# Performance work log

Measured on AMD Instinct MI355X. Metric: run time of the kernel, lower is better.

Reference implementation:

```python
import jax, jax.numpy as jnp
import numpy as np

N, E, D, H, C, G = 20000, 160000, 128, 4, 3, 512
IN_F, EF = 74, 11


def setup_inputs():
    key = jax.random.key(0)
    ks = jax.random.split(key, 20)
    rn = lambda k, shape, s=0.05: jax.random.normal(k, shape, jnp.float32) * s
    return {
        "h0": rn(ks[0], (N, IN_F), 1.0),
        "e_f": rn(ks[1], (E, EF), 1.0),
        "src": jax.random.randint(ks[2], (E,), 0, N, jnp.int32),
        "dst": jax.random.randint(ks[3], (E,), 0, N, jnp.int32),
        "node_gid": jnp.sort(jax.random.randint(ks[4], (N,), 0, G, jnp.int32)),
        "num_graphs": G,
        "lin0_W": rn(ks[5], (H, IN_F, D)),
        "lin_W": rn(ks[6], (C - 1, H, D, D)),
        "We_W": rn(ks[7], (C, H, EF, D)),
        "Wq_W": rn(ks[8], (C, H, D, D)),
        "Wk_W": rn(ks[9], (C, H, D, D)),
        "Wv_W": rn(ks[10], (C, H, D, D)),
        "ln_g": jnp.ones((C, H, D), jnp.float32),
        "ln_b": jnp.zeros((C, H, D), jnp.float32),
        "out_W": rn(ks[11], (C, H * D, D)),
        "out_b": jnp.zeros((C, D), jnp.float32),
        "proj_W": rn(ks[12], (IN_F, D)),
        "proj_b": jnp.zeros((D,), jnp.float32),
        "gru_Wih0": rn(ks[13], (2, D, 3 * D)),
        "gru_Whh0": rn(ks[14], (2, D, 3 * D)),
        "gru_bih0": jnp.zeros((2, 3 * D), jnp.float32),
        "gru_bhh0": jnp.zeros((2, 3 * D), jnp.float32),
        "gru_Wih1": rn(ks[15], (2, 2 * D, 3 * D)),
        "gru_Whh1": rn(ks[16], (2, D, 3 * D)),
        "gru_bih1": jnp.zeros((2, 3 * D), jnp.float32),
        "gru_bhh1": jnp.zeros((2, 3 * D), jnp.float32),
    }


def _seg_mean(x, ids, n):
    s = jax.ops.segment_sum(x, ids, num_segments=n)
    c = jax.ops.segment_sum(jnp.ones((x.shape[0], 1), x.dtype), ids, num_segments=n)
    return s / jnp.maximum(c, 1.0)


def _layernorm(x, g, b, eps=1e-5):
    m = jnp.mean(x, -1, keepdims=True)
    v = jnp.var(x, -1, keepdims=True)
    return (x - m) * jax.lax.rsqrt(v + eps) * g + b


def _gat_head(h, ef_raw, src, dst, n, Wl, We, Wq, Wk, Wv, g, b):
    z = h @ Wl                                  # [N, D]
    ef = ef_raw @ We                            # [E, D]
    x = jnp.stack([z[src], z[dst], ef], axis=1)  # [E, 3, D]
    Q = jnp.einsum('eid,df->eif', x, Wq)
    K = jnp.einsum('eid,df->eif', x, Wk)
    V = jnp.einsum('eid,df->eif', x, Wv)
    attn = jax.nn.softmax(jnp.einsum('eid,ejd->eij', Q, K), axis=-1)  # [E,3,3]
    m = jnp.einsum('eij,ejd->ed', attn, V)      # (attn @ V).sum(1)
    h_new = _seg_mean(m, dst, n)                # mean over incoming edges
    return _layernorm(jax.nn.relu(h_new), g, b)


def _gru_dir(xs, Wih, Whh, bih, bhh, reverse):
    # xs: [T, B, in]; torch gate order r, z, n
    def step(h, x):
        gi = x @ Wih + bih
        gh = h @ Whh + bhh
        ir, iz, inn = jnp.split(gi, 3, axis=-1)
        hr, hz, hn = jnp.split(gh, 3, axis=-1)
        r = jax.nn.sigmoid(ir + hr)
        zg = jax.nn.sigmoid(iz + hz)
        ng = jnp.tanh(inn + r * hn)
        h_new = (1.0 - zg) * ng + zg * h
        return h_new, h_new
    h0 = jnp.zeros((xs.shape[1], Whh.shape[0]), xs.dtype)
    hT, ys = jax.lax.scan(step, h0, xs, reverse=reverse)
    return hT, ys


def _forward(h0, e_f, lin0_W, lin_W, We_W, Wq_W, Wk_W, Wv_W, ln_g, ln_b,
             out_W, out_b, proj_W, proj_b,
             gru_Wih0, gru_Whh0, gru_bih0, gru_bhh0,
             gru_Wih1, gru_Whh1, gru_bih1, gru_bhh1,
             src, dst, node_gid, num_graphs):
    n = h0.shape[0]
    conv_nums, head_nums = We_W.shape[0], We_W.shape[1]
    gru_list = [_seg_mean(h0, node_gid, num_graphs)]
    h = h0
    for j in range(conv_nums):
        heads = [_gat_head(h, e_f, src, dst, n,
                           lin0_W[i] if j == 0 else lin_W[j - 1, i],
                           We_W[j, i], Wq_W[j, i], Wk_W[j, i], Wv_W[j, i],
                           ln_g[j, i], ln_b[j, i])
                 for i in range(head_nums)]
        h = jnp.concatenate(heads, axis=1) @ out_W[j] + out_b[j]
        gru_list.append(_seg_mean(h, node_gid, num_graphs))
    # GRU readout: project initial 74-dim readout, seq = [proj, h1..hC]
    x0 = gru_list[0] @ proj_W + proj_b
    seq = jnp.stack([x0] + gru_list[1:], axis=0)  # [T, G, D]
    hf0, yf0 = _gru_dir(seq, gru_Wih0[0], gru_Whh0[0], gru_bih0[0], gru_bhh0[0], False)
    hb0, yb0 = _gru_dir(seq, gru_Wih0[1], gru_Whh0[1], gru_bih0[1], gru_bhh0[1], True)
    seq1 = jnp.concatenate([yf0, yb0], axis=-1)   # [T, G, 2D]
    hf1, _ = _gru_dir(seq1, gru_Wih1[0], gru_Whh1[0], gru_bih1[0], gru_bhh1[0], False)
    hb1, _ = _gru_dir(seq1, gru_Wih1[1], gru_Whh1[1], gru_bih1[1], gru_bhh1[1], True)
    # torch returns sum over the [num_layers*2, G, D] final hidden stack
    return hf0 + hb0 + hf1 + hb1


def reference(h0, e_f, src, dst, node_gid, num_graphs, lin0_W, lin_W, We_W,
              Wq_W, Wk_W, Wv_W, ln_g, ln_b, out_W, out_b, proj_W, proj_b,
              gru_Wih0, gru_Whh0, gru_bih0, gru_bhh0,
              gru_Wih1, gru_Whh1, gru_bih1, gru_bhh1):
    return _forward(h0, e_f, lin0_W, lin_W, We_W, Wq_W, Wk_W, Wv_W, ln_g, ln_b,
                    out_W, out_b, proj_W, proj_b,
                    gru_Wih0, gru_Whh0, gru_bih0, gru_bhh0,
                    gru_Wih1, gru_Whh1, gru_bih1, gru_bhh1,
                    src, dst, node_gid, num_graphs)
```

## Files before the change

kernel.cpp:

```cpp
#include <hip/hip_runtime.h>
#include <cstdint>

#define D_   128
#define H_   4
#define C_   3
#define G_   512
#define INF_ 74
#define EF_  11
#define T_   4
#define NW_  48

typedef __attribute__((ext_vector_type(8))) short bf16x8;
typedef __attribute__((ext_vector_type(4))) float f32x4;

__device__ inline unsigned short f2bf(float x) {
  unsigned u = __float_as_uint(x);
  unsigned r = u + 0x7fffu + ((u >> 16) & 1u);
  return (unsigned short)(r >> 16);
}
__device__ inline float bf2f(unsigned short x) {
  return __uint_as_float(((unsigned)x) << 16);
}
__device__ inline void unpack8(uint4 u, float* f) {
  f[0] = __uint_as_float(u.x << 16); f[1] = __uint_as_float(u.x & 0xffff0000u);
  f[2] = __uint_as_float(u.y << 16); f[3] = __uint_as_float(u.y & 0xffff0000u);
  f[4] = __uint_as_float(u.z << 16); f[5] = __uint_as_float(u.z & 0xffff0000u);
  f[6] = __uint_as_float(u.w << 16); f[7] = __uint_as_float(u.w & 0xffff0000u);
}

struct WDesc { const float* src; unsigned short* dst; int K; int D; int trans; };
struct WPack { WDesc d[NW_]; };

__global__ __launch_bounds__(256) void k_wcvt(WPack wp)
{
  WDesc w = wp.d[blockIdx.y];
  int tot = w.K * w.D;
  for (int i = blockIdx.x * 256 + threadIdx.x; i < tot; i += gridDim.x * 256) {
    if (w.trans) {
      int d = i / w.K, k = i - d * w.K;
      w.dst[i] = f2bf(w.src[(size_t)k * w.D + d]);
    } else {
      w.dst[i] = f2bf(w.src[i]);
    }
  }
}

__global__ __launch_bounds__(256) void k_bcw(
    const float* __restrict__ GqT, const float* __restrict__ GcT,
    unsigned short* __restrict__ UTBt)
{
  int ch = blockIdx.x;
  unsigned short* dst = UTBt + (size_t)ch * 49152 + 32768;
  const float* gq = GqT + (size_t)ch * EF_ * 128;
  const float* gc = GcT + (size_t)ch * EF_ * 128;
  for (int i = threadIdx.x; i < 16384; i += 256) {
    int r = i >> 7, k = i & 127;
    float v = (r < EF_) ? gq[r * 128 + k]
            : (r < 2 * EF_) ? gc[(r - EF_) * 128 + k] : 0.f;
    dst[i] = f2bf(v);
  }
}

template <typename AT>
__global__ __launch_bounds__(256) void k_mfma(
    const AT* __restrict__ A, int lda, int aOffZ, int M, int K,
    const unsigned short* __restrict__ Bt, int btOffY, int btOffZ,
    float* __restrict__ outF, int ldc, int cOffY, int cOffZ,
    const float* __restrict__ bias,
    unsigned short* __restrict__ outH, int hStride, int hOffY, int hOffZ)
{
  const int bx = blockIdx.x, by = blockIdx.y, bz = blockIdx.z;
  A += (size_t)bz * aOffZ;
  const unsigned short* Bp = Bt + (size_t)by * btOffY + (size_t)bz * btOffZ;
  const int rowBase = bx * 128;
  __shared__ unsigned short As[128][40];
  __shared__ unsigned short Bs[128][40];
  const int t = threadIdx.x;
  const int w = t >> 6, l = t & 63;
  const int wr = w >> 1, wc = w & 1;
  const int fr = l & 15, fq = l >> 4;
  f32x4 acc[4][4];
#pragma unroll
  for (int m = 0; m < 4; m++)
#pragma unroll
    for (int n = 0; n < 4; n++) acc[m][n] = (f32x4){0.f, 0.f, 0.f, 0.f};

  const int sr = t >> 1, sh = t & 1;
  const int arow = rowBase + sr;
  const AT* aBase = A + (size_t)arow * lda;

  for (int k0 = 0; k0 < K; k0 += 32) {
    int kb = k0 + sh * 16;
    if constexpr (sizeof(AT) == 4) {
      unsigned short tmp[16];
      if (arow < M && kb + 16 <= K) {
        const AT* ap = aBase + kb;
#pragma unroll
        for (int i = 0; i < 16; i++) tmp[i] = f2bf(ap[i]);
      } else {
#pragma unroll
        for (int i = 0; i < 16; i++) {
          int gk = kb + i;
          float v = (arow < M && gk < K) ? (float)aBase[gk] : 0.f;
          tmp[i] = f2bf(v);
        }
      }
      *(uint4*)&As[sr][sh * 16]     = *(const uint4*)&tmp[0];
      *(uint4*)&As[sr][sh * 16 + 8] = *(const uint4*)&tmp[8];
    } else {
      if (arow < M && kb + 16 <= K) {
        const unsigned short* ap = (const unsigned short*)aBase + kb;
        *(uint4*)&As[sr][sh * 16]     = *(const uint4*)(ap);
        *(uint4*)&As[sr][sh * 16 + 8] = *(const uint4*)(ap + 8);
      } else {
#pragma unroll
        for (int i = 0; i < 16; i++) {
          int gk = kb + i;
          As[sr][sh * 16 + i] = (arow < M && gk < K)
              ? ((const unsigned short*)aBase)[gk] : (unsigned short)0;
        }
      }
    }
    if (t < 128) {
      unsigned short tmp[32];
      if (k0 + 32 <= K) {
        const unsigned short* bp = Bp + (size_t)t * K + k0;
#pragma unroll
        for (int i = 0; i < 32; i++) tmp[i] = bp[i];
      } else {
#pragma unroll
        for (int i = 0; i < 32; i++) {
          int gk = k0 + i;
          tmp[i] = (gk < K) ? Bp[(size_t)t * K + gk] : (unsigned short)0;
        }
      }
#pragma unroll
      for (int i = 0; i < 4; i++) *(uint4*)&Bs[t][i * 8] = *(const uint4*)&tmp[i * 8];
    }
    __syncthreads();
    bf16x8 af[4], bfr[4];
#pragma unroll
    for (int m = 0; m < 4; m++) af[m]  = *(const bf16x8*)&As[wr * 64 + m * 16 + fr][fq * 8];
#pragma unroll
    for (int n = 0; n < 4; n++) bfr[n] = *(const bf16x8*)&Bs[wc * 64 + n * 16 + fr][fq * 8];
#pragma unroll
    for (int m = 0; m < 4; m++)
#pragma unroll
      for (int n = 0; n < 4; n++)
        acc[m][n] = __builtin_amdgcn_mfma_f32_16x16x32_bf16(af[m], bfr[n], acc[m][n], 0, 0, 0);
    __syncthreads();
  }
#pragma unroll
  for (int m = 0; m < 4; m++) {
    int row0 = rowBase + wr * 64 + m * 16 + fq * 4;
#pragma unroll
    for (int n = 0; n < 4; n++) {
      int col = wc * 64 + n * 16 + fr;
#pragma unroll
      for (int r = 0; r < 4; r++) {
        int row = row0 + r;
        if (row < M) {
          float v = acc[m][n][r];
          if (outH) {
            outH[(size_t)row * hStride + by * hOffY + bz * hOffZ + col] = f2bf(v);
          } else {
            if (bias) v += bias[col];
            outF[(size_t)row * ldc + by * cOffY + bz * cOffZ + col] = v;
          }
        }
      }
    }
  }
}

__global__ void k_hist(const int* __restrict__ dst, int* __restrict__ deg, int E)
{
  int e = blockIdx.x * blockDim.x + threadIdx.x;
  if (e < E) atomicAdd(&deg[dst[e]], 1);
}

__global__ __launch_bounds__(1024) void k_scan(const int* __restrict__ deg,
                                               int* __restrict__ rowp, int N)
{
  __shared__ int part[1024];
  int t = threadIdx.x;
  int chunk = (N + 1023) / 1024;
  int base = t * chunk;
  int s = 0;
  for (int i = 0; i < chunk; i++) { int idx = base + i; if (idx < N) s += deg[idx]; }
  part[t] = s;
  __syncthreads();
  for (int off = 1; off < 1024; off <<= 1) {
    int v = (t >= off) ? part[t - off] : 0;
    __syncthreads();
    part[t] += v;
    __syncthreads();
  }
  int run = part[t] - s;
  for (int i = 0; i < chunk; i++) {
    int idx = base + i;
    if (idx < N) { rowp[idx] = run; run += deg[idx]; }
  }
  if (t == 1023) rowp[N] = part[1023];
}

__global__ void k_fill(const int* __restrict__ src, const int* __restrict__ dst,
                       const int* __restrict__ rowp, int* __restrict__ cursor,
                       int* __restrict__ eids, int* __restrict__ src_perm,
                       int* __restrict__ dst_perm, int E)
{
  int e = blockIdx.x * blockDim.x + threadIdx.x;
  if (e < E) {
    int d = dst[e];
    int pos = atomicAdd(&cursor[d], 1);
    int slot = rowp[d] + pos;
    eids[slot] = e;
    src_perm[slot] = src[e];
    dst_perm[slot] = d;
  }
}

__global__ void k_efperm(const float* __restrict__ e_f, const int* __restrict__ eids,
                         float* __restrict__ ef_perm, int E)
{
  int i = blockIdx.x * blockDim.x + threadIdx.x;
  if (i < E * EF_) {
    int idx = i / EF_, f = i - idx * EF_;
    ef_perm[i] = e_f[(size_t)eids[idx] * EF_ + f];
  }
}

__global__ __launch_bounds__(128) void k_small(
    const float* __restrict__ WeW, const float* __restrict__ WqW,
    const float* __restrict__ WkW, const float* __restrict__ WvW,
    float* __restrict__ WeQ, float* __restrict__ WeK, float* __restrict__ WeV,
    float* __restrict__ M2, float* __restrict__ GqT, float* __restrict__ GcT)
{
  int ch = blockIdx.x;
  const float* We = WeW + (size_t)ch * EF_ * 128;
  const float* Wq = WqW + (size_t)ch * 128 * 128;
  const float* Wk = WkW + (size_t)ch * 128 * 128;
  const float* Wv = WvW + (size_t)ch * 128 * 128;
  __shared__ float sWe[EF_ * 128], sQ[EF_ * 128], sK[EF_ * 128];
  int d = threadIdx.x;
  for (int i = d; i < EF_ * 128; i += 128) sWe[i] = We[i];
  __syncthreads();
  for (int f = 0; f < EF_; f++) {
    float aq = 0.f, ak = 0.f, av = 0.f;
    for (int k = 0; k < 128; k++) {
      float w = sWe[f * 128 + k];
      aq += w * Wq[k * 128 + d];
      ak += w * Wk[k * 128 + d];
      av += w * Wv[k * 128 + d];
    }
    WeQ[(size_t)ch * EF_ * 128 + f * 128 + d] = aq;
    WeK[(size_t)ch * EF_ * 128 + f * 128 + d] = ak;
    WeV[(size_t)ch * EF_ * 128 + f * 128 + d] = av;
    sQ[f * 128 + d] = aq;
    sK[f * 128 + d] = ak;
  }
  __syncthreads();
  if (d < EF_ * EF_) {
    int a = d / EF_, b = d % EF_;
    float s = 0.f;
    for (int k = 0; k < 128; k++) s += sQ[a * 128 + k] * sK[b * 128 + k];
    M2[(size_t)ch * (EF_ * EF_) + d] = s;
  }
  for (int f = 0; f < EF_; f++) {
    float aq = 0.f, ac = 0.f;
    for (int k = 0; k < 128; k++) {
      aq += Wq[(size_t)d * 128 + k] * sK[f * 128 + k];
      ac += Wk[(size_t)d * 128 + k] * sQ[f * 128 + k];
    }
    GqT[(size_t)ch * EF_ * 128 + f * 128 + d] = aq;
    GcT[(size_t)ch * EF_ * 128 + f * 128 + d] = ac;
  }
}

__global__ __launch_bounds__(128) void k_wve(
    const float* __restrict__ WvW, const float* __restrict__ WeV,
    unsigned short* __restrict__ WvE)
{
  int ch = blockIdx.x;
  const float* Wv  = WvW + (size_t)ch * 16384;
  const float* wev = WeV + (size_t)ch * EF_ * 128;
  unsigned short* dst = WvE + (size_t)ch * 20480;
  for (int i = threadIdx.x; i < 20480; i += 128) {
    int d = i / 160, k = i - d * 160;
    float v = (k < 128) ? Wv[(size_t)k * 128 + d]
            : (k < 128 + EF_) ? wev[(size_t)(k - 128) * 128 + d] : 0.f;
    dst[i] = f2bf(v);
  }
}

__global__ __launch_bounds__(256) void k_ss(
    const unsigned short* __restrict__ Zb, const unsigned short* __restrict__ UTb,
    float* __restrict__ ss, int N)
{
  int h = threadIdx.x >> 6, lane = threadIdx.x & 63;
  int n = blockIdx.x;
  unsigned uz = *(const unsigned*)(Zb + (size_t)n * 512 + h * 128 + 2 * lane);
  unsigned uu = *(const unsigned*)(UTb + (size_t)n * 1536 + h * 384 + 2 * lane);
  float zx = __uint_as_float(uz << 16), zy = __uint_as_float(uz & 0xffff0000u);
  float ux = __uint_as_float(uu << 16), uy = __uint_as_float(uu & 0xffff0000u);
  float p = zx * ux + zy * uy;
#pragma unroll
  for (int m = 32; m; m >>= 1) p += __shfl_xor(p, m, 64);
  if (lane == 0) ss[n * H_ + h] = p;
}

__global__ __launch_bounds__(256) void k_elog(
    const unsigned short* __restrict__ UTb, const float* __restrict__ ss,
    const float* __restrict__ M2, const float* __restrict__ ef_perm,
    const int* __restrict__ src_perm, const int* __restrict__ dst_perm,
    float* __restrict__ elog, int E, int layer)
{
  int i0 = blockIdx.x * 64;
  __shared__ float efs[64 * EF_];
  __shared__ float m2s[4 * EF_ * EF_];
  int t = threadIdx.x;
  for (int i = t; i < 64 * EF_; i += 256) {
    int gi = i0 * EF_ + i;
    efs[i] = (gi < E * EF_) ? ef_perm[gi] : 0.f;
  }
  for (int i = t; i < 4 * EF_ * EF_; i += 256)
    m2s[i] = M2[(size_t)layer * 4 * EF_ * EF_ + i];
  __syncthreads();
  int sl = t >> 2, h = t & 3;
  int idx = i0 + sl;
  if (idx < E) {
    int s = src_perm[idx], d = dst_perm[idx];
    const float* ef = &efs[sl * EF_];
    const float* m2 = &m2s[h * EF_ * EF_];
    float ee = 0.f;
#pragma unroll
    for (int a = 0; a < EF_; a++) {
      float r = 0.f;
#pragma unroll
      for (int b = 0; b < EF_; b++) r += m2[a * EF_ + b] * ef[b];
      ee += ef[a] * r;
    }
    const unsigned short* bs = UTb + (size_t)s * 1536 + h * 384 + 256;
    const unsigned short* cs = bs + EF_;
    const unsigned short* bd = UTb + (size_t)d * 1536 + h * 384 + 256;
    const unsigned short* cd = bd + EF_;
    float se = 0.f, es = 0.f, de = 0.f, ed = 0.f;
#pragma unroll
    for (int f = 0; f < EF_; f++) {
      float e = ef[f];
      se += bf2f(bs[f]) * e;
      es += bf2f(cs[f]) * e;
      de += bf2f(bd[f]) * e;
      ed += bf2f(cd[f]) * e;
    }
    float* o = elog + ((size_t)idx * H_ + h) * 6;
    o[0] = ss[s * H_ + h];
    o[1] = se; o[2] = de; o[3] = es; o[4] = ed; o[5] = ee;
  }
}

__global__ __launch_bounds__(256) void k_edge(
    const unsigned short* __restrict__ Zb, const unsigned short* __restrict__ UTb,
    const float* __restrict__ ss, const float* __restrict__ elog,
    const float* __restrict__ ef_perm, const int* __restrict__ rowp,
    const int* __restrict__ src_perm, unsigned short* __restrict__ aggZE, int N)
{
  const int h = threadIdx.x >> 6;
  const int lane = threadIdx.x & 63;
  const int q = lane & 15;
  const int g = lane >> 4;
  const int lb = lane & 48;
  const int n = blockIdx.x;

  float zd[8], ud[8], td[8];
  unpack8(*(const uint4*)(Zb + (size_t)n * 512 + h * 128 + q * 8), zd);
  const unsigned short* utp = UTb + (size_t)n * 1536 + h * 384 + q * 8;
  unpack8(*(const uint4*)(utp), ud);
  unpack8(*(const uint4*)(utp + 128), td);
  const float ssd = ss[n * H_ + h];
  const int beg = rowp[n], end = rowp[n + 1];
  float acc[8];
#pragma unroll
  for (int i = 0; i < 8; i++) acc[i] = 0.f;
  float wdsum = 0.f, a11 = 0.f;

  for (int idx0 = beg; idx0 < end; idx0 += 4) {
    int idxg = idx0 + g;
    bool act = idxg < end;
    int idxc = act ? idxg : beg;
    int s = src_perm[idxc];
    float zs[8];
    unpack8(*(const uint4*)(Zb + (size_t)s * 512 + h * 128 + q * 8), zs);
    float v1 = 0.f, v2 = 0.f;
#pragma unroll
    for (int i = 0; i < 8; i++) {
      v1 += zs[i] * ud[i];
      v2 += zs[i] * td[i];
    }
#pragma unroll
    for (int m = 1; m < 16; m <<= 1) {
      v1 += __shfl_xor(v1, m, 64);
      v2 += __shfl_xor(v2, m, 64);
    }
    float lv = (q < 6) ? elog[((size_t)idxc * H_ + h) * 6 + q] : 0.f;
    float S00 = __shfl(lv, lb + 0, 64);
    float S02 = __shfl(lv, lb + 1, 64);
    float S12 = __shfl(lv, lb + 2, 64);
    float S20 = __shfl(lv, lb + 3, 64);
    float S21 = __shfl(lv, lb + 4, 64);
    float S22 = __shfl(lv, lb + 5, 64);
    float m0 = fmaxf(fmaxf(S00, v1), S02);
    float e00 = __expf(S00 - m0), e01 = __expf(v1 - m0), e02 = __expf(S02 - m0);
    float i0r = 1.f / (e00 + e01 + e02);
    float m1 = fmaxf(fmaxf(v2, ssd), S12);
    float e10 = __expf(v2 - m1), e11 = __expf(ssd - m1), e12 = __expf(S12 - m1);
    float i1r = 1.f / (e10 + e11 + e12);
    float m2 = fmaxf(fmaxf(S20, S21), S22);
    float e20 = __expf(S20 - m2), e21 = __expf(S21 - m2), e22 = __expf(S22 - m2);
    float i2r = 1.f / (e20 + e21 + e22);
    float w0 = e00 * i0r + e10 * i1r + e20 * i2r;
    float w1 = e01 * i0r + e11 * i1r + e21 * i2r;
    float w2 = e02 * i0r + e12 * i1r + e22 * i2r;
    if (!act) { w0 = 0.f; w1 = 0.f; w2 = 0.f; }
#pragma unroll
    for (int i = 0; i < 8; i++) acc[i] += w0 * zs[i];
    wdsum += w1;
    float efl = (q < EF_) ? ef_perm[(size_t)idxc * EF_ + q] : 0.f;
    a11 += w2 * efl;
  }
#pragma unroll
  for (int m = 16; m < 64; m <<= 1) {
#pragma unroll
    for (int i = 0; i < 8; i++) acc[i] += __shfl_xor(acc[i], m, 64);
    wdsum += __shfl_xor(wdsum, m, 64);
    a11 += __shfl_xor(a11, m, 64);
  }
  int cnt = end - beg;
  float invc = (cnt > 0) ? 1.f / (float)cnt : 1.f;
  unsigned short* ob = aggZE + (size_t)n * 640 + h * 160;
  if (g == 0) {
    unsigned short tmp[8];
#pragma unroll
    for (int i = 0; i < 8; i++) tmp[i] = f2bf((acc[i] + wdsum * zd[i]) * invc);
    *(uint4*)(ob + q * 8) = *(const uint4*)&tmp[0];
    ob[128 + q] = (q < EF_) ? f2bf(a11 * invc) : (unsigned short)0;
  } else if (g == 1) {
    ob[144 + q] = 0;
  }
}

__global__ __launch_bounds__(256) void k_ln(
    float* __restrict__ zh, const float* __restrict__ lng,
    const float* __restrict__ lnb, int N, int layer)
{
  int h = threadIdx.x >> 6, lane = threadIdx.x & 63;
  int n = blockIdx.x;
  float* p = zh + (size_t)n * 512 + h * 128 + 2 * lane;
  float2 v = *(const float2*)p;
  v.x = fmaxf(v.x, 0.f); v.y = fmaxf(v.y, 0.f);
  float s1 = v.x + v.y;
#pragma unroll
  for (int m = 32; m; m >>= 1) s1 += __shfl_xor(s1, m, 64);
  float mean = s1 * (1.f / 128.f);
  float dx = v.x - mean, dy = v.y - mean;
  float s2 = dx * dx + dy * dy;
#pragma unroll
  for (int m = 32; m; m >>= 1) s2 += __shfl_xor(s2, m, 64);
  float rstd = rsqrtf(s2 * (1.f / 128.f) + 1e-5f);
  int gi = (layer * H_ + h) * 128 + 2 * lane;
  float2 g2 = *(const float2*)&lng[gi];
  float2 b2 = *(const float2*)&lnb[gi];
  float2 o;
  o.x = dx * rstd * g2.x + b2.x;
  o.y = dy * rstd * g2.y + b2.y;
  *(float2*)p = o;
}

__global__ void k_gmean(const float* __restrict__ X, const int* __restrict__ gid,
                        float* __restrict__ outp, int N, int ld)
{
  int g = blockIdx.x;
  int lo = 0, hi = N;
  while (lo < hi) { int m = (lo + hi) >> 1; if (gid[m] < g) lo = m + 1; else hi = m; }
  int s0 = lo;
  lo = s0; hi = N;
  while (lo < hi) { int m = (lo + hi) >> 1; if (gid[m] < g + 1) lo = m + 1; else hi = m; }
  int s1 = lo;
  float inv = 1.f / (float)((s1 - s0) > 0 ? (s1 - s0) : 1);
  for (int d = threadIdx.x; d < ld; d += blockDim.x) {
    float s = 0.f;
    for (int n = s0; n < s1; n++) s += X[(size_t)n * ld + d];
    outp[(size_t)g * ld + d] = s * inv;
  }
}

__global__ __launch_bounds__(128) void k_gru(
    const float* __restrict__ seq, int inDim,
    const float* __restrict__ Wih, const float* __restrict__ Whh,
    const float* __restrict__ bih, const float* __restrict__ bhh,
    float* __restrict__ yout, float* __restrict__ hfinal)
{
  int g = blockIdx.x, dir = blockIdx.y, d = threadIdx.x;
  const float* Wih_d = Wih + (size_t)dir * inDim * 384;
  const float* Whh_d = Whh + (size_t)dir * 128 * 384;
  const float* bih_d = bih + dir * 384;
  const float* bhh_d = bhh + dir * 384;
  __shared__ float xb[256];
  __shared__ float hb[128];
  float h = 0.f;
  for (int st = 0; st < T_; st++) {
    int t = dir ? (T_ - 1 - st) : st;
    for (int k = d; k < inDim; k += 128) xb[k] = seq[((size_t)t * G_ + g) * inDim + k];
    hb[d] = h;
    __syncthreads();
    float gr = bih_d[d], gz = bih_d[128 + d], gn = bih_d[256 + d];
    for (int k = 0; k < inDim; k++) {
      float xv = xb[k];
      const float* wr = Wih_d + (size_t)k * 384;
      gr += xv * wr[d];
      gz += xv * wr[128 + d];
      gn += xv * wr[256 + d];
    }
    float hr = bhh_d[d], hz = bhh_d[128 + d], hn = bhh_d[256 + d];
    for (int k = 0; k < 128; k++) {
      float hv = hb[k];
      const float* wr = Whh_d + (size_t)k * 384;
      hr += hv * wr[d];
      hz += hv * wr[128 + d];
      hn += hv * wr[256 + d];
    }
    float r  = 1.f / (1.f + __expf(-(gr + hr)));
    float zg = 1.f / (1.f + __expf(-(gz + hz)));
    float ng = tanhf(gn + r * hn);
    h = (1.f - zg) * ng + zg * h;
    if (yout) yout[((size_t)t * G_ + g) * 256 + dir * 128 + d] = h;
    __syncthreads();
  }
  hfinal[((size_t)dir * G_ + g) * 128 + d] = h;
}

__global__ void k_final(const float* __restrict__ fp, float* __restrict__ outp, int n)
{
  int i = blockIdx.x * blockDim.x + threadIdx.x;
  if (i < n) {
    outp[i] = fp[i] + fp[G_ * 128 + i] + fp[2 * G_ * 128 + i] + fp[3 * G_ * 128 + i];
  }
}

extern "C" void kernel_launch(void* const* d_in, const int* in_sizes, int n_in,
                              void* d_out, int out_size, void* d_ws, size_t ws_size,
                              hipStream_t stream)
{
  (void)n_in; (void)ws_size;
  const float* h0   = (const float*)d_in[0];
  const float* e_f  = (const float*)d_in[1];
  const int*   srcI = (const int*)d_in[2];
  const int*   dstI = (const int*)d_in[3];
  const int*   gid  = (const int*)d_in[4];
  const float* lin0 = (const float*)d_in[6];
  const float* linW = (const float*)d_in[7];
  const float* WeW  = (const float*)d_in[8];
  const float* WqW  = (const float*)d_in[9];
  const float* WkW  = (const float*)d_in[10];
  const float* WvW  = (const float*)d_in[11];
  const float* lng  = (const float*)d_in[12];
  const float* lnb  = (const float*)d_in[13];
  const float* outW = (const float*)d_in[14];
  const float* outb = (const float*)d_in[15];
  const float* projW= (const float*)d_in[16];
  const float* projb= (const float*)d_in[17];
  const float* Wih0 = (const float*)d_in[18];
  const float* Whh0 = (const float*)d_in[19];
  const float* bih0 = (const float*)d_in[20];
  const float* bhh0 = (const float*)d_in[21];
  const float* Wih1 = (const float*)d_in[22];
  const float* Whh1 = (const float*)d_in[23];
  const float* bih1 = (const float*)d_in[24];
  const float* bhh1 = (const float*)d_in[25];
  float* outp = (float*)d_out;

  const int N = in_sizes[0] / INF_;
  const int E = in_sizes[2];

  char* wp = (char*)d_ws;
  auto alloc = [&](size_t bytes) -> void* {
    void* p = (void*)wp;
    wp += (bytes + 255) & ~(size_t)255;
    return p;
  };
  unsigned short* Zb  = (unsigned short*)alloc((size_t)N * 512 * 2);
  unsigned short* UTb = (unsigned short*)alloc((size_t)N * 1536 * 2);
  unsigned short* aggZE = (unsigned short*)alloc((size_t)N * 640 * 2);
  float* zh   = (float*)alloc((size_t)N * 512 * 4);
  float* hcur = (float*)alloc((size_t)N * 128 * 4);
  float* ssb  = (float*)alloc((size_t)N * H_ * 4);
  float* elog = (float*)alloc((size_t)E * H_ * 6 * 4);
  float* efp  = (float*)alloc((size_t)E * EF_ * 4);
  float* WeQ  = (float*)alloc((size_t)C_ * H_ * EF_ * 128 * 4);
  float* WeK  = (float*)alloc((size_t)C_ * H_ * EF_ * 128 * 4);
  float* WeV  = (float*)alloc((size_t)C_ * H_ * EF_ * 128 * 4);
  float* M2   = (float*)alloc((size_t)C_ * H_ * EF_ * EF_ * 4);
  float* GqT  = (float*)alloc((size_t)C_ * H_ * EF_ * 128 * 4);
  float* GcT  = (float*)alloc((size_t)C_ * H_ * EF_ * 128 * 4);
  float* Mbuf = (float*)alloc((size_t)C_ * H_ * 16384 * 4);
  unsigned short* WkPl  = (unsigned short*)alloc((size_t)C_ * H_ * 16384 * 2);
  unsigned short* UTBt  = (unsigned short*)alloc((size_t)C_ * H_ * 3 * 16384 * 2);
  unsigned short* WvE   = (unsigned short*)alloc((size_t)C_ * H_ * 20480 * 2);
  unsigned short* linBt0 = (unsigned short*)alloc((size_t)4 * 128 * INF_ * 2);
  unsigned short* linBt12= (unsigned short*)alloc((size_t)2 * 512 * 128 * 2);
  unsigned short* outBt  = (unsigned short*)alloc((size_t)C_ * 128 * 512 * 2);
  unsigned short* projBt = (unsigned short*)alloc((size_t)128 * INF_ * 2);
  int* deg    = (int*)alloc((size_t)N * 4);
  int* cursor = (int*)alloc((size_t)N * 4);
  int* rowp   = (int*)alloc((size_t)(N + 1) * 4);
  int* eids   = (int*)alloc((size_t)E * 4);
  int* srcp   = (int*)alloc((size_t)E * 4);
  int* dstp   = (int*)alloc((size_t)E * 4);
  float* gm74 = (float*)alloc((size_t)G_ * INF_ * 4);
  float* seq  = (float*)alloc((size_t)T_ * G_ * 128 * 4);
  float* seq1 = (float*)alloc((size_t)T_ * G_ * 256 * 4);
  float* fparts=(float*)alloc((size_t)4 * G_ * 128 * 4);

  const int gM = (N + 127) / 128;

  hipMemsetAsync(deg, 0, (size_t)N * 4, stream);
  hipMemsetAsync(cursor, 0, (size_t)N * 4, stream);
  k_hist<<<(E + 255) / 256, 256, 0, stream>>>(dstI, deg, E);
  k_scan<<<1, 1024, 0, stream>>>(deg, rowp, N);
  k_fill<<<(E + 255) / 256, 256, 0, stream>>>(srcI, dstI, rowp, cursor,
                                              eids, srcp, dstp, E);
  k_efperm<<<(E * EF_ + 255) / 256, 256, 0, stream>>>(e_f, eids, efp, E);

  k_small<<<C_ * H_, 128, 0, stream>>>(WeW, WqW, WkW, WvW, WeQ, WeK, WeV, M2,
                                       GqT, GcT);
  k_wve<<<C_ * H_, 128, 0, stream>>>(WvW, WeV, WvE);

  {
    WPack w{};
    int nw = 0;
    auto addw = [&](const float* s, unsigned short* d, int K, int D, int tr) {
      w.d[nw].src = s; w.d[nw].dst = d; w.d[nw].K = K; w.d[nw].D = D;
      w.d[nw].trans = tr; nw++;
    };
    for (int h = 0; h < 4; h++)
      addw(lin0 + (size_t)h * INF_ * 128, linBt0 + (size_t)h * 128 * INF_, INF_, 128, 1);
    for (int j = 1; j < 3; j++)
      for (int h = 0; h < 4; h++)
        addw(linW + ((size_t)(j - 1) * 4 + h) * 16384,
             linBt12 + (size_t)(j - 1) * 65536 + (size_t)h * 16384, 128, 128, 1);
    for (int j = 0; j < 3; j++)
      addw(outW + (size_t)j * 65536, outBt + (size_t)j * 65536, 512, 128, 1);
    addw(projW, projBt, INF_, 128, 1);
    for (int ch = 0; ch < 12; ch++)
      addw(WkW + (size_t)ch * 16384, WkPl + (size_t)ch * 16384, 128, 128, 0);
    k_wcvt<<<dim3(64, nw), 256, 0, stream>>>(w);
  }

  k_mfma<float><<<dim3(1, 1, 12), 256, 0, stream>>>(
      WqW, 128, 16384, 128, 128, WkPl, 0, 16384,
      Mbuf, 128, 0, 16384, nullptr, nullptr, 0, 0, 0);

  {
    WPack w{};
    int nw = 0;
    for (int ch = 0; ch < 12; ch++) {
      w.d[nw++] = { Mbuf + (size_t)ch * 16384, UTBt + (size_t)ch * 49152,
                    128, 128, 0 };
      w.d[nw++] = { Mbuf + (size_t)ch * 16384, UTBt + (size_t)ch * 49152 + 16384,
                    128, 128, 1 };
    }
    k_wcvt<<<dim3(64, nw), 256, 0, stream>>>(w);
    k_bcw<<<12, 256, 0, stream>>>(GqT, GcT, UTBt);
  }

  k_gmean<<<G_, 128, 0, stream>>>(h0, gid, gm74, N, INF_);
  k_mfma<float><<<dim3(4, 1, 1), 256, 0, stream>>>(
      gm74, INF_, 0, G_, INF_, projBt, 0, 0,
      seq, 128, 0, 0, projb, nullptr, 0, 0, 0);

  for (int j = 0; j < C_; j++) {
    if (j == 0)
      k_mfma<float><<<dim3(gM, 4, 1), 256, 0, stream>>>(
          h0, INF_, 0, N, INF_, linBt0, 128 * INF_, 0,
          nullptr, 0, 0, 0, nullptr, Zb, 512, 128, 0);
    else
      k_mfma<float><<<dim3(gM, 4, 1), 256, 0, stream>>>(
          hcur, 128, 0, N, 128, linBt12 + (size_t)(j - 1) * 65536, 16384, 0,
          nullptr, 0, 0, 0, nullptr, Zb, 512, 128, 0);
    k_mfma<unsigned short><<<dim3(gM, 3, 4), 256, 0, stream>>>(
        Zb, 512, 128, N, 128, UTBt + (size_t)j * 4 * 49152, 16384, 49152,
        nullptr, 0, 0, 0, nullptr, UTb, 1536, 128, 384);
    k_ss<<<N, 256, 0, stream>>>(Zb, UTb, ssb, N);
    k_elog<<<(E + 63) / 64, 256, 0, stream>>>(UTb, ssb, M2, efp, srcp, dstp,
                                              elog, E, j);
    k_edge<<<N, 256, 0, stream>>>(Zb, UTb, ssb, elog, efp, rowp, srcp, aggZE, N);
    k_mfma<unsigned short><<<dim3(gM, 1, 4), 256, 0, stream>>>(
        aggZE, 640, 160, N, 160, WvE + (size_t)j * 4 * 20480, 0, 20480,
        zh, 512, 0, 128, nullptr, nullptr, 0, 0, 0);
    k_ln<<<N, 256, 0, stream>>>(zh, lng, lnb, N, j);
    k_mfma<float><<<dim3(gM, 1, 1), 256, 0, stream>>>(
        zh, 512, 0, N, 512, outBt + (size_t)j * 65536, 0, 0,
        hcur, 128, 0, 0, outb + j * 128, nullptr, 0, 0, 0);
    k_gmean<<<G_, 128, 0, stream>>>(hcur, gid, seq + (size_t)(j + 1) * G_ * 128, N, 128);
  }

  k_gru<<<dim3(G_, 2), 128, 0, stream>>>(seq, 128, Wih0, Whh0, bih0, bhh0,
                                         seq1, fparts);
  k_gru<<<dim3(G_, 2), 128, 0, stream>>>(seq1, 256, Wih1, Whh1, bih1, bhh1,
                                         nullptr, fparts + 2 * G_ * 128);
  k_final<<<(out_size + 255) / 256, 256, 0, stream>>>(fparts, outp, out_size);
}
```

Before: 1.392 ms.

## Hoist GRU input projections into batched MFMA GEMM and widen recurrent kernel

Computes the GRU input-to-hidden projections for all timesteps and both directions at once with the existing bf16 MFMA GEMM, instead of per-step scalar loops inside the recurrent kernel. The recurrent kernel now uses 384 threads, one per gate output, and only does the hidden-to-hidden matvec plus the gate math, with shared-memory exchange between gates. This removes redundant serial FLOPs from the latency-bound recurrence. It adds bf16 rounding of the input weights, an extra workspace buffer, and more barriers per step.

```diff
diff --git a/kernel.cpp b/kernel.cpp
--- a/kernel.cpp
+++ b/kernel.cpp
@@ -494,49 +494,41 @@
   }
 }
 
-__global__ __launch_bounds__(128) void k_gru(
-    const float* __restrict__ seq, int inDim,
-    const float* __restrict__ Wih, const float* __restrict__ Whh,
+__global__ __launch_bounds__(384) void k_gruR(
+    const float* __restrict__ gi, const float* __restrict__ Whh,
     const float* __restrict__ bih, const float* __restrict__ bhh,
     float* __restrict__ yout, float* __restrict__ hfinal)
 {
-  int g = blockIdx.x, dir = blockIdx.y, d = threadIdx.x;
-  const float* Wih_d = Wih + (size_t)dir * inDim * 384;
-  const float* Whh_d = Whh + (size_t)dir * 128 * 384;
-  const float* bih_d = bih + dir * 384;
-  const float* bhh_d = bhh + dir * 384;
-  __shared__ float xb[256];
+  const int g = blockIdx.x, dir = blockIdx.y, t = threadIdx.x;
+  const float* W = Whh + (size_t)dir * 128 * 384 + t;
+  const float bi = bih[dir * 384 + t];
+  const float bh = bhh[dir * 384 + t];
   __shared__ float hb[128];
-  float h = 0.f;
+  __shared__ float rb[128], zb[128], nb[128];
+  if (t < 128) hb[t] = 0.f;
+  __syncthreads();
   for (int st = 0; st < T_; st++) {
-    int t = dir ? (T_ - 1 - st) : st;
-    for (int k = d; k < inDim; k += 128) xb[k] = seq[((size_t)t * G_ + g) * inDim + k];
-    hb[d] = h;
+    int ts = dir ? (T_ - 1 - st) : st;
+    float acc = bh;
+    for (int k = 0; k < 128; k++) acc += hb[k] * W[(size_t)k * 384];
+    float gv = gi[((size_t)ts * G_ + g) * 768 + dir * 384 + t] + bi;
+    if (t < 128) {
+      rb[t] = 1.f / (1.f + __expf(-(gv + acc)));
+    } else if (t < 256) {
+      zb[t - 128] = 1.f / (1.f + __expf(-(gv + acc)));
+    }
     __syncthreads();
-    float gr = bih_d[d], gz = bih_d[128 + d], gn = bih_d[256 + d];
-    for (int k = 0; k < inDim; k++) {
-      float xv = xb[k];
-      const float* wr = Wih_d + (size_t)k * 384;
-      gr += xv * wr[d];
-      gz += xv * wr[128 + d];
-      gn += xv * wr[256 + d];
-    }
-    float hr = bhh_d[d], hz = bhh_d[128 + d], hn = bhh_d[256 + d];
-    for (int k = 0; k < 128; k++) {
-      float hv = hb[k];
-      const float* wr = Whh_d + (size_t)k * 384;
-      hr += hv * wr[d];
-      hz += hv * wr[128 + d];
-      hn += hv * wr[256 + d];
-    }
-    float r  = 1.f / (1.f + __expf(-(gr + hr)));
-    float zg = 1.f / (1.f + __expf(-(gz + hz)));
-    float ng = tanhf(gn + r * hn);
-    h = (1.f - zg) * ng + zg * h;
-    if (yout) yout[((size_t)t * G_ + g) * 256 + dir * 128 + d] = h;
+    if (t >= 256) nb[t - 256] = tanhf(gv + rb[t - 256] * acc);
     __syncthreads();
-  }
-  hfinal[((size_t)dir * G_ + g) * 128 + d] = h;
+    if (t < 128) {
+      float z = zb[t];
+      float h = (1.f - z) * nb[t] + z * hb[t];
+      hb[t] = h;
+      if (yout) yout[((size_t)ts * G_ + g) * 256 + dir * 128 + t] = h;
+    }
+    __syncthreads();
+  }
+  if (t < 128) hfinal[((size_t)dir * G_ + g) * 128 + t] = hb[t];
 }
 
 __global__ void k_final(const float* __restrict__ fp, float* __restrict__ outp, int n)
@@ -610,6 +602,9 @@
   unsigned short* linBt12= (unsigned short*)alloc((size_t)2 * 512 * 128 * 2);
   unsigned short* outBt  = (unsigned short*)alloc((size_t)C_ * 128 * 512 * 2);
   unsigned short* projBt = (unsigned short*)alloc((size_t)128 * INF_ * 2);
+  unsigned short* WihBt0 = (unsigned short*)alloc((size_t)768 * 128 * 2);
+  unsigned short* WihBt1 = (unsigned short*)alloc((size_t)768 * 256 * 2);
+  float* gibuf = (float*)alloc((size_t)T_ * G_ * 768 * 4);
   int* deg    = (int*)alloc((size_t)N * 4);
   int* cursor = (int*)alloc((size_t)N * 4);
   int* rowp   = (int*)alloc((size_t)(N + 1) * 4);
@@ -653,6 +648,12 @@
     addw(projW, projBt, INF_, 128, 1);
     for (int ch = 0; ch < 12; ch++)
       addw(WkW + (size_t)ch * 16384, WkPl + (size_t)ch * 16384, 128, 128, 0);
+    for (int dir = 0; dir < 2; dir++) {
+      addw(Wih0 + (size_t)dir * 128 * 384, WihBt0 + (size_t)dir * 384 * 128,
+           128, 384, 1);
+      addw(Wih1 + (size_t)dir * 256 * 384, WihBt1 + (size_t)dir * 384 * 256,
+           256, 384, 1);
+    }
     k_wcvt<<<dim3(64, nw), 256, 0, stream>>>(w);
   }
 
@@ -704,9 +705,15 @@
     k_gmean<<<G_, 128, 0, stream>>>(hcur, gid, seq + (size_t)(j + 1) * G_ * 128, N, 128);
   }
 
-  k_gru<<<dim3(G_, 2), 128, 0, stream>>>(seq, 128, Wih0, Whh0, bih0, bhh0,
-                                         seq1, fparts);
-  k_gru<<<dim3(G_, 2), 128, 0, stream>>>(seq1, 256, Wih1, Whh1, bih1, bhh1,
-                                         nullptr, fparts + 2 * G_ * 128);
+  k_mfma<float><<<dim3(16, 6, 1), 256, 0, stream>>>(
+      seq, 128, 0, T_ * G_, 128, WihBt0, 128 * 128, 0,
+      gibuf, 768, 128, 0, nullptr, nullptr, 0, 0, 0);
+  k_gruR<<<dim3(G_, 2), 384, 0, stream>>>(gibuf, Whh0, bih0, bhh0,
+                                          seq1, fparts);
+  k_mfma<float><<<dim3(16, 6, 1), 256, 0, stream>>>(
+      seq1, 256, 0, T_ * G_, 256, WihBt1, 128 * 256, 0,
+      gibuf, 768, 128, 0, nullptr, nullptr, 0, 0, 0);
+  k_gruR<<<dim3(G_, 2), 384, 0, stream>>>(gibuf, Whh1, bih1, bhh1,
+                                          nullptr, fparts + 2 * G_ * 128);
   k_final<<<(out_size + 255) / 256, 256, 0, stream>>>(fparts, outp, out_size);
 }
```

Measured after the change: 1.334 ms. 1.04x faster.
